# Kernel tuning notes

Hardware: AMD Instinct MI355X
Metric: run time of the kernel (lower is better)

The kernel has to match this reference:

```python
import jax, jax.numpy as jnp
import numpy as np

B, C, H, W = 4, 256, 64, 64
HALF = C // 2
BN_EPS = 1e-5


def setup_inputs() -> dict:
    key = jax.random.key(0)
    ks = jax.random.split(key, 6)
    scale = 1.0 / np.sqrt(C)
    return {
        "x": jax.random.normal(ks[0], (B, C, H, W), dtype=jnp.float32),
        "w1": jax.random.normal(ks[1], (HALF, C), dtype=jnp.float32) * scale,
        "w2": jax.random.normal(ks[2], (HALF, C), dtype=jnp.float32) * scale,
        "w3": jax.random.normal(ks[3], (HALF, C), dtype=jnp.float32) * scale,
        "w4": jax.random.normal(ks[4], (C, HALF), dtype=jnp.float32) * (1.0 / np.sqrt(HALF)),
        "gamma": jnp.ones((C,), dtype=jnp.float32),
        "beta": jnp.zeros((C,), dtype=jnp.float32),
        "running_mean": jnp.zeros((C,), dtype=jnp.float32),
        "running_var": jnp.ones((C,), dtype=jnp.float32),
    }


def _conv1x1(x, w):
    # x: [b,c,h,w], w: [out,in] -> [b,out,h,w]
    return jnp.einsum('bchw,oc->bohw', x, w)


def reference(x, w1, w2, w3, w4, gamma, beta, running_mean, running_var):
    b, Cin, h, w = x.shape
    c = Cin // 2
    hw = h * w
    n1 = _conv1x1(x, w1)  # [b,c,h,w]
    n2 = _conv1x1(x, w2)
    n3 = _conv1x1(x, w3)
    # Faithful to torch .view (raw reshape, NOT a transpose)
    q = n1.reshape(b, hw, c)   # [b,hw,c]
    k = n2.reshape(b, c, hw)   # [b,c,hw]
    attn = jnp.einsum('bic,bcj->bij', q, k)        # [b,hw,hw]
    attn = jax.nn.softmax(attn, axis=-1)
    v = n3.reshape(b, hw, c)
    res = jnp.einsum('bij,bjc->bic', attn, v)      # [b,hw,c]
    res = res.reshape(b, c, h, w)
    out = _conv1x1(res, w4)                        # [b,C,h,w]
    # BatchNorm2d in eval mode with running stats
    inv = jax.lax.rsqrt(running_var + BN_EPS)
    out = (out - running_mean[None, :, None, None]) * (gamma * inv)[None, :, None, None] + beta[None, :, None, None]
    return out + x
```

## Files before the change

### kernel.cpp

```cpp
#include <hip/hip_runtime.h>
#include <cstdint>

#define BN 4
#define CIN 256
#define HALFC 128
#define HW 4096
#define SPLIT 4
#define JT 64
#define JITERS (HW / SPLIT / JT)

typedef float  floatx4 __attribute__((ext_vector_type(4)));
typedef short  shortx8 __attribute__((ext_vector_type(8)));

#if __has_builtin(__builtin_amdgcn_exp2f)
#define EXP2F(x) __builtin_amdgcn_exp2f(x)
#else
#define EXP2F(x) exp2f(x)
#endif
#define L2E 1.44269504088896f

__device__ __forceinline__ unsigned short f2bf(float f) {
  unsigned u = __float_as_uint(f);
  u += 0x7FFFu + ((u >> 16) & 1u);
  return (unsigned short)(u >> 16);
}

__device__ __forceinline__ void async16(const void* g, void* l) {
  __builtin_amdgcn_global_load_lds((const __attribute__((address_space(1))) void*)g,
                                   (__attribute__((address_space(3))) void*)l, 16, 0, 0);
}

__global__ __launch_bounds__(256) void k_split(const float* __restrict__ x,
    const float* __restrict__ w1, const float* __restrict__ w2,
    const float* __restrict__ w3, unsigned short* __restrict__ Xth,
    unsigned short* __restrict__ Wh) {
  __shared__ float smf[64 * 65];
  int bid = blockIdx.x;
  int t = threadIdx.x;
  if (bid < 1024) {
    int b = bid >> 8, rem = bid & 255;
    int cit = rem >> 6, pxt = rem & 63;
    const float* src = x + (size_t)b * 1048576 + (size_t)(cit * 64) * HW + pxt * 64;
#pragma unroll
    for (int k = 0; k < 16; k++) {
      int idx = k * 256 + t;
      int r = idx >> 6, c = idx & 63;
      smf[r * 65 + c] = src[(size_t)r * HW + c];
    }
    __syncthreads();
    int prow = t >> 2, seg = t & 3;
    union { unsigned short us[16]; uint4 v[2]; } oh;
#pragma unroll
    for (int u = 0; u < 16; u++)
      oh.us[u] = f2bf(smf[(seg * 16 + u) * 65 + prow]);
    size_t dst = (size_t)b * 1048576 + (size_t)(pxt * 64 + prow) * 256 + cit * 64 + seg * 16;
    *(uint4*)(Xth + dst) = oh.v[0];
    *(uint4*)(Xth + dst + 8) = oh.v[1];
  } else {
    int bw = bid - 1024;
    int f0 = bw * 8192 + t * 32;
    const float* wsrc;
    int fo;
    if (f0 < 32768)      { wsrc = w1; fo = f0; }
    else if (f0 < 65536) { wsrc = w2; fo = f0 - 32768; }
    else                 { wsrc = w3; fo = f0 - 65536; }
    union { unsigned short us[32]; uint4 v[4]; } oh;
#pragma unroll
    for (int u = 0; u < 32; u++) oh.us[u] = f2bf(wsrc[fo + u]);
#pragma unroll
    for (int k = 0; k < 4; k++) *((uint4*)(Wh + f0) + k) = oh.v[k];
  }
}

__global__ __launch_bounds__(256) void k_projM(const unsigned short* __restrict__ Xth,
    const unsigned short* __restrict__ Wh, unsigned short* __restrict__ Q,
    unsigned short* __restrict__ Kt, unsigned short* __restrict__ n3) {
  __shared__ unsigned short XhS[4096];
  __shared__ unsigned short ES[9216];
  int bid = blockIdx.x;
  int pxt = bid & 31;
  int ct = bid >> 5;
  int b = ct / 6, cot = ct % 6;
  int px0 = pxt * 128, co0 = cot * 64;
  int t = threadIdx.x;
  int w = t >> 6, lane = t & 63, l16 = lane & 15, quad = lane >> 4;

  int myco = co0 + w * 16 + l16;
  shortx8 whf[8];
#pragma unroll
  for (int s = 0; s < 8; s++)
    whf[s] = *(const shortx8*)(Wh + (size_t)myco * 256 + s * 32 + quad * 8);
  floatx4 acc[8];
  floatx4 zf = {0.f, 0.f, 0.f, 0.f};
#pragma unroll
  for (int mt = 0; mt < 8; mt++) acc[mt] = zf;
  const unsigned short* XhB = Xth + (size_t)b * 1048576;
  int k8 = lane >> 4, pxm = lane & 15;

#pragma unroll
  for (int s = 0; s < 8; s++) {
    __syncthreads();
#pragma unroll
    for (int c2 = 0; c2 < 2; c2++) {
      int px = px0 + (c2 * 4 + w) * 16 + pxm;
      async16(XhB + (size_t)px * 256 + s * 32 + k8 * 8, (char*)XhS + c2 * 4096 + w * 1024);
    }
    __syncthreads();
#pragma unroll
    for (int mt = 0; mt < 8; mt++) {
      shortx8 ah = *(const shortx8*)((const char*)XhS + mt * 1024 + lane * 16);
      acc[mt] = __builtin_amdgcn_mfma_f32_16x16x32_bf16(ah, whf[s], acc[mt], 0, 0, 0);
    }
  }
  __syncthreads();
  if (cot < 2 || cot >= 4) {
    int co_l = w * 16 + l16;
#pragma unroll
    for (int mt = 0; mt < 8; mt++) {
      int px = mt * 16 + quad * 4;
      unsigned lo = (unsigned)f2bf(acc[mt][0]) | ((unsigned)f2bf(acc[mt][1]) << 16);
      unsigned hi = (unsigned)f2bf(acc[mt][2]) | ((unsigned)f2bf(acc[mt][3]) << 16);
      *(uint2*)(ES + co_l * 136 + px) = make_uint2(lo, hi);
    }
    __syncthreads();
    int cr = t >> 2, seg = t & 3;
    unsigned short* dstb = (cot < 2)
        ? Q  + (size_t)b * 524288 + (size_t)(co0 + cr) * HW
        : n3 + (size_t)b * 524288 + (size_t)(co0 - 256 + cr) * HW;
#pragma unroll
    for (int k2 = 0; k2 < 4; k2++) {
      uint4 v = *(const uint4*)(ES + cr * 136 + seg * 32 + k2 * 8);
      *(uint4*)(dstb + px0 + seg * 32 + k2 * 8) = v;
    }
  } else {
#pragma unroll
    for (int mt = 0; mt < 8; mt++)
#pragma unroll
      for (int rr = 0; rr < 4; rr++) {
        int px = mt * 16 + quad * 4 + rr;
        ES[px * 72 + w * 16 + l16] = f2bf(acc[mt][rr]);
      }
    __syncthreads();
    int ch0 = co0 - 128;
#pragma unroll
    for (int it = 0; it < 4; it++) {
      int cid = it * 256 + t;
      int px = cid >> 3, c8 = cid & 7;
      uint4 v = *(const uint4*)(ES + px * 72 + c8 * 8);
      *(uint4*)(Kt + (size_t)b * 524288 + (size_t)(px0 + px) * 128 + ch0 + c8 * 8) = v;
    }
  }
}

__global__ __launch_bounds__(256) void k_layoutVF(const unsigned short* __restrict__ n3,
    unsigned short* __restrict__ VtF) {
  __shared__ unsigned short sm[8192];
  int bid = blockIdx.x;
  int b = bid >> 6, jt = bid & 63;
  int t = threadIdx.x;
  const unsigned short* src = n3 + (size_t)b * 524288 + (size_t)(jt * 2) * 4096;
#pragma unroll
  for (int k = 0; k < 32; k++) sm[k * 256 + t] = src[k * 256 + t];
  __syncthreads();
  unsigned short* dst = VtF + (size_t)b * 524288 + (size_t)jt * 8192;
#pragma unroll
  for (int k = 0; k < 4; k++) {
    int s = k * 256 + t;
    int nt = s >> 7, kt = (s >> 6) & 1, quad = (s >> 4) & 3, l16 = s & 15;
    union { unsigned short us[8]; uint4 v; } o;
#pragma unroll
    for (int e = 0; e < 8; e++)
      o.us[e] = sm[kt * 4096 + (quad * 8 + e) * 128 + nt * 16 + l16];
    *(uint4*)(dst + s * 8) = o.v;
  }
}

__global__ __launch_bounds__(256, 2) void k_flash(const unsigned short* __restrict__ Q,
    const unsigned short* __restrict__ Kt, const unsigned short* __restrict__ VtF,
    float* __restrict__ Opart, float* __restrict__ ml) {
  __shared__ unsigned short KtS[2 * 8192];
  __shared__ unsigned short PS[4 * 32 * 64];
  int bid0 = blockIdx.x;
  int bid = (bid0 & 7) * 64 + (bid0 >> 3);
  int itile = bid & 31, sp = (bid >> 5) & 3, b = bid >> 7;
  int t = threadIdx.x;
  int w = t >> 6, lane = t & 63, l16 = lane & 15, quad = lane >> 4;
  int i0 = itile * 128;

  shortx8 qf[2][4];
#pragma unroll
  for (int ig = 0; ig < 2; ig++) {
    const unsigned short* qp = Q + ((size_t)b * HW + i0 + w * 32 + ig * 16 + l16) * 128 + quad * 8;
#pragma unroll
    for (int ks = 0; ks < 4; ks++) qf[ig][ks] = *(const shortx8*)(qp + ks * 32);
  }
  __asm__ __volatile__("s_waitcnt vmcnt(0)" ::: "memory");

  floatx4 O[2][8];
  floatx4 zf = {0.f, 0.f, 0.f, 0.f};
#pragma unroll
  for (int ig = 0; ig < 2; ig++)
#pragma unroll
    for (int nt = 0; nt < 8; nt++) O[ig][nt] = zf;
  float m_i[2] = {-1e30f, -1e30f}, l_i[2] = {0.f, 0.f};

  int ccK = w * 4 + quad;
  const unsigned short* kbase = Kt + (size_t)b * HW * 128
                              + (size_t)(sp * 1024 + l16) * 128 + ccK * 8;
  const unsigned short* vB = VtF + (size_t)b * 524288 + (size_t)(sp * 16) * 8192 + lane * 8;
  char* Pw = (char*)PS + w * 4096;

#pragma unroll
  for (int c4 = 0; c4 < 4; c4++)
    async16(kbase + c4 * 2048, (char*)KtS + c4 * 4096 + w * 1024);

  for (int it = 0; it < JITERS; it++) {
    int cur = it & 1, nxt = cur ^ 1;
    __asm__ __volatile__("s_barrier" ::: "memory");
    shortx8 vf[8][2];
    {
      const unsigned short* vt = vB + (size_t)it * 8192;
#pragma unroll
      for (int nt = 0; nt < 8; nt++)
#pragma unroll
        for (int kt = 0; kt < 2; kt++)
          vf[nt][kt] = *(const shortx8*)(vt + (nt * 2 + kt) * 512);
    }
    if (it + 1 < JITERS) {
      const unsigned short* kp = kbase + (size_t)(it + 1) * 8192;
#pragma unroll
      for (int c4 = 0; c4 < 4; c4++)
        async16(kp + c4 * 2048, (char*)KtS + nxt * 16384 + c4 * 4096 + w * 1024);
      __asm__ __volatile__("s_waitcnt vmcnt(20)" ::: "memory");
    } else {
      __asm__ __volatile__("s_waitcnt vmcnt(16)" ::: "memory");
    }
    __asm__ __volatile__("s_barrier" ::: "memory");

    const char* kc = (const char*)KtS + cur * 16384;

    floatx4 S[2][4];
#pragma unroll
    for (int ig = 0; ig < 2; ig++)
#pragma unroll
      for (int mt = 0; mt < 4; mt++) S[ig][mt] = zf;
    __builtin_amdgcn_s_setprio(1);
#pragma unroll
    for (int mt = 0; mt < 4; mt++) {
#pragma unroll
      for (int ks = 0; ks < 4; ks++) {
        shortx8 af = *(const shortx8*)(kc + mt * 4096 + ks * 1024 + lane * 16);
        S[0][mt] = __builtin_amdgcn_mfma_f32_16x16x32_bf16(af, qf[0][ks], S[0][mt], 0, 0, 0);
        S[1][mt] = __builtin_amdgcn_mfma_f32_16x16x32_bf16(af, qf[1][ks], S[1][mt], 0, 0, 0);
      }
    }
    __builtin_amdgcn_s_setprio(0);

    float tmax[2];
#pragma unroll
    for (int ig = 0; ig < 2; ig++) {
      float a0 = fmaxf(fmaxf(S[ig][0][0], S[ig][0][1]), fmaxf(S[ig][0][2], S[ig][0][3]));
      float a1 = fmaxf(fmaxf(S[ig][1][0], S[ig][1][1]), fmaxf(S[ig][1][2], S[ig][1][3]));
      float a2 = fmaxf(fmaxf(S[ig][2][0], S[ig][2][1]), fmaxf(S[ig][2][2], S[ig][2][3]));
      float a3 = fmaxf(fmaxf(S[ig][3][0], S[ig][3][1]), fmaxf(S[ig][3][2], S[ig][3][3]));
      float tm = fmaxf(fmaxf(a0, a1), fmaxf(a2, a3));
      tm = fmaxf(tm, __shfl_xor(tm, 16));
      tm = fmaxf(tm, __shfl_xor(tm, 32));
      tmax[ig] = tm;
    }
    float alpha[2] = {1.f, 1.f};
    if (__ballot(tmax[0] > m_i[0] + 8.f || tmax[1] > m_i[1] + 8.f)) {
#pragma unroll
      for (int ig = 0; ig < 2; ig++) {
        float mn = fmaxf(m_i[ig], tmax[ig]);
        alpha[ig] = EXP2F((m_i[ig] - mn) * L2E);
        m_i[ig] = mn;
        float ar[4];
#pragma unroll
        for (int rr = 0; rr < 4; rr++) ar[rr] = __shfl(alpha[ig], quad * 4 + rr);
#pragma unroll
        for (int nt = 0; nt < 8; nt++)
#pragma unroll
          for (int rr = 0; rr < 4; rr++) O[ig][nt][rr] *= ar[rr];
      }
    }
#pragma unroll
    for (int ig = 0; ig < 2; ig++) {
      float nsc = m_i[ig] * L2E;
      float sm[4];
#pragma unroll
      for (int mt = 0; mt < 4; mt++) {
        float p0 = EXP2F(fmaf(S[ig][mt][0], L2E, -nsc));
        float p1 = EXP2F(fmaf(S[ig][mt][1], L2E, -nsc));
        float p2 = EXP2F(fmaf(S[ig][mt][2], L2E, -nsc));
        float p3 = EXP2F(fmaf(S[ig][mt][3], L2E, -nsc));
        S[ig][mt][0] = p0; S[ig][mt][1] = p1; S[ig][mt][2] = p2; S[ig][mt][3] = p3;
        sm[mt] = (p0 + p1) + (p2 + p3);
      }
      float ts = (sm[0] + sm[1]) + (sm[2] + sm[3]);
      ts += __shfl_xor(ts, 16);
      ts += __shfl_xor(ts, 32);
      l_i[ig] = l_i[ig] * alpha[ig] + ts;
#pragma unroll
      for (int mt = 0; mt < 4; mt++) {
        unsigned lo = __builtin_amdgcn_perm(__float_as_uint(S[ig][mt][1]),
                                            __float_as_uint(S[ig][mt][0]), 0x07060302u);
        unsigned hi = __builtin_amdgcn_perm(__float_as_uint(S[ig][mt][3]),
                                            __float_as_uint(S[ig][mt][2]), 0x07060302u);
        *(uint2*)(Pw + ig * 2048 + (mt * 2 + (quad >> 1)) * 256 + l16 * 16 + (quad & 1) * 8)
            = make_uint2(lo, hi);
      }
    }
    __asm__ __volatile__("s_waitcnt lgkmcnt(0)" ::: "memory");
    if (it + 1 < JITERS) {
      __asm__ __volatile__("s_waitcnt vmcnt(4)" ::: "memory");
    } else {
      __asm__ __volatile__("s_waitcnt vmcnt(0)" ::: "memory");
    }
    __builtin_amdgcn_s_setprio(1);
#pragma unroll
    for (int kt = 0; kt < 2; kt++) {
      shortx8 pf0 = *(const shortx8*)(Pw + kt * 1024 + lane * 16);
      shortx8 pf1 = *(const shortx8*)(Pw + 2048 + kt * 1024 + lane * 16);
#pragma unroll
      for (int nt = 0; nt < 8; nt++) {
        O[0][nt] = __builtin_amdgcn_mfma_f32_16x16x32_bf16(pf0, vf[nt][kt], O[0][nt], 0, 0, 0);
        O[1][nt] = __builtin_amdgcn_mfma_f32_16x16x32_bf16(pf1, vf[nt][kt], O[1][nt], 0, 0, 0);
      }
    }
    __builtin_amdgcn_s_setprio(0);
  }
#pragma unroll
  for (int ig = 0; ig < 2; ig++) {
    float* Ob = Opart + ((size_t)(sp * 4 + b) * HW + i0 + w * 32 + ig * 16) * 128;
#pragma unroll
    for (int nt = 0; nt < 8; nt++)
#pragma unroll
      for (int rr = 0; rr < 4; rr++)
        Ob[(size_t)(quad * 4 + rr) * 128 + nt * 16 + l16] = O[ig][nt][rr];
  }
  if (quad == 0) {
    float2* mlp = (float2*)ml;
#pragma unroll
    for (int ig = 0; ig < 2; ig++)
      mlp[(size_t)(sp * 4 + b) * HW + i0 + w * 32 + ig * 16 + l16]
          = make_float2(m_i[ig], l_i[ig]);
  }
}

__global__ __launch_bounds__(256) void k_merge(const float* __restrict__ Opart,
    const float* __restrict__ ml, float* __restrict__ res) {
  size_t e = (size_t)blockIdx.x * 256 + threadIdx.x;
  int cq = (int)(e & 31);
  int i = (int)((e >> 5) & 4095);
  int b = (int)(e >> 17);
  const float2* mlp = (const float2*)ml;
  float m[SPLIT], l[SPLIT];
  float M = -1e30f;
#pragma unroll
  for (int s = 0; s < SPLIT; s++) {
    float2 st = mlp[(size_t)(s * 4 + b) * HW + i];
    m[s] = st.x; l[s] = st.y;
    M = fmaxf(M, m[s]);
  }
  float denom = 0.f;
  float wgt[SPLIT];
#pragma unroll
  for (int s = 0; s < SPLIT; s++) {
    float ws_ = EXP2F((m[s] - M) * L2E);
    wgt[s] = ws_;
    denom += l[s] * ws_;
  }
  float inv = 1.f / denom;
  floatx4 acc = {0.f, 0.f, 0.f, 0.f};
#pragma unroll
  for (int s = 0; s < SPLIT; s++) {
    floatx4 v = *(const floatx4*)(Opart + ((size_t)(s * 4 + b) * HW + i) * 128 + cq * 4);
    acc += v * (wgt[s] * inv);
  }
  *(floatx4*)(res + e * 4) = acc;
}

__global__ __launch_bounds__(256) void k_out(const float* __restrict__ res,
    const float* __restrict__ w4, const float* __restrict__ gamma,
    const float* __restrict__ beta, const float* __restrict__ rmean,
    const float* __restrict__ rvar, const float* __restrict__ x,
    float* __restrict__ out) {
  __shared__ float wt[16 * 128];
  int bid = blockIdx.x;
  int cot = bid & 15;
  int st = (bid >> 4) & 15;
  int b = bid >> 8;
  int t = threadIdx.x;
  int co0 = cot * 16;
#pragma unroll
  for (int k = 0; k < 8; k++) wt[k * 256 + t] = w4[(size_t)co0 * 128 + k * 256 + t];
  __syncthreads();
  int px = st * 256 + t;
  const float* rb = res + (size_t)b * 524288 + px;
  float acc[16];
#pragma unroll
  for (int r = 0; r < 16; r++) acc[r] = 0.f;
  for (int ci = 0; ci < 128; ci += 4) {
    float xv[4];
#pragma unroll
    for (int kk = 0; kk < 4; kk++) xv[kk] = rb[(size_t)(ci + kk) * HW];
#pragma unroll
    for (int r = 0; r < 16; r++) {
      floatx4 wv = *(const floatx4*)&wt[r * 128 + ci];
#pragma unroll
      for (int kk = 0; kk < 4; kk++) acc[r] += wv[kk] * xv[kk];
    }
  }
  const float* xb = x + ((size_t)b * 256 + co0) * HW + px;
  float* ob = out + ((size_t)b * 256 + co0) * HW + px;
#pragma unroll
  for (int r = 0; r < 16; r++) {
    int co = co0 + r;
    float g = gamma[co] * rsqrtf(rvar[co] + 1e-5f);
    float bb = beta[co] - rmean[co] * g;
    ob[(size_t)r * HW] = acc[r] * g + bb + xb[(size_t)r * HW];
  }
}

extern "C" void kernel_launch(void* const* d_in, const int* in_sizes, int n_in,
                              void* d_out, int out_size, void* d_ws, size_t ws_size,
                              hipStream_t stream) {
  const float* x     = (const float*)d_in[0];
  const float* w1    = (const float*)d_in[1];
  const float* w2    = (const float*)d_in[2];
  const float* w3    = (const float*)d_in[3];
  const float* w4    = (const float*)d_in[4];
  const float* gamma = (const float*)d_in[5];
  const float* beta  = (const float*)d_in[6];
  const float* rmean = (const float*)d_in[7];
  const float* rvar  = (const float*)d_in[8];
  float* out = (float*)d_out;
  char* ws = (char*)d_ws;

  size_t off = (size_t)SPLIT * 4 * HW * 128 * 4;
  float* Opart = (float*)ws;
  unsigned short* n3  = (unsigned short*)ws;
  unsigned short* Xth = (unsigned short*)(ws + ((size_t)8 << 20));
  unsigned short* Q   = (unsigned short*)(ws + off); off += (size_t)4 * HW * 128 * 2;
  unsigned short* Kt  = (unsigned short*)(ws + off); off += (size_t)4 * HW * 128 * 2;
  unsigned short* VtF = (unsigned short*)(ws + off); off += (size_t)4 * HW * 128 * 2;
  float* ml  = (float*)(ws + off); off += (size_t)SPLIT * 4 * HW * 2 * 4;
  float* res = (float*)(ws + off); off += (size_t)4 * HW * 128 * 4;
  unsigned short* Wh = (unsigned short*)(ws + off); off += (size_t)384 * 256 * 2;
  if (ws_size < off) return;

  k_split   <<<1036, 256, 0, stream>>>(x, w1, w2, w3, Xth, Wh);
  k_projM   <<<768,  256, 0, stream>>>(Xth, Wh, Q, Kt, n3);
  k_layoutVF<<<256,  256, 0, stream>>>(n3, VtF);
  k_flash   <<<512,  256, 0, stream>>>(Q, Kt, VtF, Opart, ml);
  k_merge   <<<2048, 256, 0, stream>>>(Opart, ml, res);
  k_out     <<<1024, 256, 0, stream>>>(res, w4, gamma, beta, rmean, rvar, x, out);
}
```

Measured before the change: 191.2 us.

## Software-pipeline flash loop so previous P·V MFMAs overlap current QK and softmax

Moves the body of the attention loop into an inlined helper and unrolls the loop by two. Each step now runs the P·V product for the previous key tile while the current tile's V fragments load and before its QK scores and softmax. The P tile and V register fragments are double-buffered, and a trailing P·V runs after the loop. The aim is to hide the wait on V loads and shared-memory P writes behind matrix work, at the cost of doubled V registers and extra LDS, which risks spills or lower occupancy.

Measured after the change: 200.5 us. +4.9%, slower.

```diff
diff --git a/kernel.cpp b/kernel.cpp
--- a/kernel.cpp
+++ b/kernel.cpp
@@ -175,11 +175,132 @@
   }
 }
 
+__device__ __forceinline__ void flash_body(int it, bool haspv,
+    shortx8 (&vfc)[8][2], shortx8 (&vfp)[8][2],
+    shortx8 (&qf)[2][4], floatx4 (&O)[2][8],
+    float (&m_i)[2], float (&l_i)[2],
+    const unsigned short* vB, const unsigned short* kbase,
+    unsigned short* KtS, char* Pw, int w, int lane, int l16, int quad) {
+  int cur = it & 1, nxt = cur ^ 1;
+  floatx4 zf = {0.f, 0.f, 0.f, 0.f};
+  __asm__ __volatile__("s_barrier" ::: "memory");
+  {
+    const unsigned short* vt = vB + (size_t)it * 8192;
+#pragma unroll
+    for (int nt = 0; nt < 8; nt++)
+#pragma unroll
+      for (int kt = 0; kt < 2; kt++)
+        vfc[nt][kt] = *(const shortx8*)(vt + (nt * 2 + kt) * 512);
+  }
+  if (it + 1 < JITERS) {
+    const unsigned short* kp = kbase + (size_t)(it + 1) * 8192;
+#pragma unroll
+    for (int c4 = 0; c4 < 4; c4++)
+      async16(kp + c4 * 2048, (char*)KtS + nxt * 16384 + c4 * 4096 + w * 1024);
+    __asm__ __volatile__("s_waitcnt vmcnt(20)" ::: "memory");
+  } else {
+    __asm__ __volatile__("s_waitcnt vmcnt(16)" ::: "memory");
+  }
+  __asm__ __volatile__("s_barrier" ::: "memory");
+
+  if (haspv) {
+    __asm__ __volatile__("s_waitcnt lgkmcnt(0)" ::: "memory");
+    const char* Pr = Pw + ((it ^ 1) & 1) * 4096;
+    __builtin_amdgcn_s_setprio(1);
+#pragma unroll
+    for (int kt = 0; kt < 2; kt++) {
+      shortx8 pf0 = *(const shortx8*)(Pr + kt * 1024 + lane * 16);
+      shortx8 pf1 = *(const shortx8*)(Pr + 2048 + kt * 1024 + lane * 16);
+#pragma unroll
+      for (int nt = 0; nt < 8; nt++) {
+        O[0][nt] = __builtin_amdgcn_mfma_f32_16x16x32_bf16(pf0, vfp[nt][kt], O[0][nt], 0, 0, 0);
+        O[1][nt] = __builtin_amdgcn_mfma_f32_16x16x32_bf16(pf1, vfp[nt][kt], O[1][nt], 0, 0, 0);
+      }
+    }
+    __builtin_amdgcn_s_setprio(0);
+  }
+
+  const char* kc = (const char*)KtS + cur * 16384;
+  floatx4 S[2][4];
+#pragma unroll
+  for (int ig = 0; ig < 2; ig++)
+#pragma unroll
+    for (int mt = 0; mt < 4; mt++) S[ig][mt] = zf;
+  __builtin_amdgcn_s_setprio(1);
+#pragma unroll
+  for (int mt = 0; mt < 4; mt++) {
+#pragma unroll
+    for (int ks = 0; ks < 4; ks++) {
+      shortx8 af = *(const shortx8*)(kc + mt * 4096 + ks * 1024 + lane * 16);
+      S[0][mt] = __builtin_amdgcn_mfma_f32_16x16x32_bf16(af, qf[0][ks], S[0][mt], 0, 0, 0);
+      S[1][mt] = __builtin_amdgcn_mfma_f32_16x16x32_bf16(af, qf[1][ks], S[1][mt], 0, 0, 0);
+    }
+  }
+  __builtin_amdgcn_s_setprio(0);
+
+  float tmax[2];
+#pragma unroll
+  for (int ig = 0; ig < 2; ig++) {
+    float a0 = fmaxf(fmaxf(S[ig][0][0], S[ig][0][1]), fmaxf(S[ig][0][2], S[ig][0][3]));
+    float a1 = fmaxf(fmaxf(S[ig][1][0], S[ig][1][1]), fmaxf(S[ig][1][2], S[ig][1][3]));
+    float a2 = fmaxf(fmaxf(S[ig][2][0], S[ig][2][1]), fmaxf(S[ig][2][2], S[ig][2][3]));
+    float a3 = fmaxf(fmaxf(S[ig][3][0], S[ig][3][1]), fmaxf(S[ig][3][2], S[ig][3][3]));
+    float tm = fmaxf(fmaxf(a0, a1), fmaxf(a2, a3));
+    tm = fmaxf(tm, __shfl_xor(tm, 16));
+    tm = fmaxf(tm, __shfl_xor(tm, 32));
+    tmax[ig] = tm;
+  }
+  float alpha[2] = {1.f, 1.f};
+  if (__ballot(tmax[0] > m_i[0] + 8.f || tmax[1] > m_i[1] + 8.f)) {
+#pragma unroll
+    for (int ig = 0; ig < 2; ig++) {
+      float mn = fmaxf(m_i[ig], tmax[ig]);
+      alpha[ig] = EXP2F((m_i[ig] - mn) * L2E);
+      m_i[ig] = mn;
+      float ar[4];
+#pragma unroll
+      for (int rr = 0; rr < 4; rr++) ar[rr] = __shfl(alpha[ig], quad * 4 + rr);
+#pragma unroll
+      for (int nt = 0; nt < 8; nt++)
+#pragma unroll
+        for (int rr = 0; rr < 4; rr++) O[ig][nt][rr] *= ar[rr];
+    }
+  }
+  char* Pd = Pw + (it & 1) * 4096;
+#pragma unroll
+  for (int ig = 0; ig < 2; ig++) {
+    float nsc = m_i[ig] * L2E;
+    float sm[4];
+#pragma unroll
+    for (int mt = 0; mt < 4; mt++) {
+      float p0 = EXP2F(fmaf(S[ig][mt][0], L2E, -nsc));
+      float p1 = EXP2F(fmaf(S[ig][mt][1], L2E, -nsc));
+      float p2 = EXP2F(fmaf(S[ig][mt][2], L2E, -nsc));
+      float p3 = EXP2F(fmaf(S[ig][mt][3], L2E, -nsc));
+      S[ig][mt][0] = p0; S[ig][mt][1] = p1; S[ig][mt][2] = p2; S[ig][mt][3] = p3;
+      sm[mt] = (p0 + p1) + (p2 + p3);
+    }
+    float ts = (sm[0] + sm[1]) + (sm[2] + sm[3]);
+    ts += __shfl_xor(ts, 16);
+    ts += __shfl_xor(ts, 32);
+    l_i[ig] = l_i[ig] * alpha[ig] + ts;
+#pragma unroll
+    for (int mt = 0; mt < 4; mt++) {
+      unsigned lo = __builtin_amdgcn_perm(__float_as_uint(S[ig][mt][1]),
+                                          __float_as_uint(S[ig][mt][0]), 0x07060302u);
+      unsigned hi = __builtin_amdgcn_perm(__float_as_uint(S[ig][mt][3]),
+                                          __float_as_uint(S[ig][mt][2]), 0x07060302u);
+      *(uint2*)(Pd + ig * 2048 + (mt * 2 + (quad >> 1)) * 256 + l16 * 16 + (quad & 1) * 8)
+          = make_uint2(lo, hi);
+    }
+  }
+}
+
 __global__ __launch_bounds__(256, 2) void k_flash(const unsigned short* __restrict__ Q,
     const unsigned short* __restrict__ Kt, const unsigned short* __restrict__ VtF,
     float* __restrict__ Opart, float* __restrict__ ml) {
   __shared__ unsigned short KtS[2 * 8192];
-  __shared__ unsigned short PS[4 * 32 * 64];
+  __shared__ unsigned short PS[4 * 2 * 2048];
   int bid0 = blockIdx.x;
   int bid = (bid0 & 7) * 64 + (bid0 >> 3);
   int itile = bid & 31, sp = (bid >> 5) & 3, b = bid >> 7;
@@ -208,127 +329,31 @@
   const unsigned short* kbase = Kt + (size_t)b * HW * 128
                               + (size_t)(sp * 1024 + l16) * 128 + ccK * 8;
   const unsigned short* vB = VtF + (size_t)b * 524288 + (size_t)(sp * 16) * 8192 + lane * 8;
-  char* Pw = (char*)PS + w * 4096;
+  char* Pw = (char*)PS + w * 8192;
 
 #pragma unroll
   for (int c4 = 0; c4 < 4; c4++)
     async16(kbase + c4 * 2048, (char*)KtS + c4 * 4096 + w * 1024);
 
-  for (int it = 0; it < JITERS; it++) {
-    int cur = it & 1, nxt = cur ^ 1;
-    __asm__ __volatile__("s_barrier" ::: "memory");
-    shortx8 vf[8][2];
-    {
-      const unsigned short* vt = vB + (size_t)it * 8192;
-#pragma unroll
-      for (int nt = 0; nt < 8; nt++)
-#pragma unroll
-        for (int kt = 0; kt < 2; kt++)
-          vf[nt][kt] = *(const shortx8*)(vt + (nt * 2 + kt) * 512);
-    }
-    if (it + 1 < JITERS) {
-      const unsigned short* kp = kbase + (size_t)(it + 1) * 8192;
-#pragma unroll
-      for (int c4 = 0; c4 < 4; c4++)
-        async16(kp + c4 * 2048, (char*)KtS + nxt * 16384 + c4 * 4096 + w * 1024);
-      __asm__ __volatile__("s_waitcnt vmcnt(20)" ::: "memory");
-    } else {
-      __asm__ __volatile__("s_waitcnt vmcnt(16)" ::: "memory");
-    }
-    __asm__ __volatile__("s_barrier" ::: "memory");
-
-    const char* kc = (const char*)KtS + cur * 16384;
-
-    floatx4 S[2][4];
-#pragma unroll
-    for (int ig = 0; ig < 2; ig++)
-#pragma unroll
-      for (int mt = 0; mt < 4; mt++) S[ig][mt] = zf;
-    __builtin_amdgcn_s_setprio(1);
-#pragma unroll
-    for (int mt = 0; mt < 4; mt++) {
-#pragma unroll
-      for (int ks = 0; ks < 4; ks++) {
-        shortx8 af = *(const shortx8*)(kc + mt * 4096 + ks * 1024 + lane * 16);
-        S[0][mt] = __builtin_amdgcn_mfma_f32_16x16x32_bf16(af, qf[0][ks], S[0][mt], 0, 0, 0);
-        S[1][mt] = __builtin_amdgcn_mfma_f32_16x16x32_bf16(af, qf[1][ks], S[1][mt], 0, 0, 0);
+  shortx8 vfA[8][2], vfB[8][2];
+#pragma unroll 1
+  for (int it2 = 0; it2 < JITERS; it2 += 2) {
+    flash_body(it2,     it2 > 0, vfA, vfB, qf, O, m_i, l_i, vB, kbase, KtS, Pw, w, lane, l16, quad);
+    flash_body(it2 + 1, true,    vfB, vfA, qf, O, m_i, l_i, vB, kbase, KtS, Pw, w, lane, l16, quad);
+  }
+  {
+    __asm__ __volatile__("s_waitcnt lgkmcnt(0)" ::: "memory");
+    const char* Pr = Pw + ((JITERS - 1) & 1) * 4096;
+#pragma unroll
+    for (int kt = 0; kt < 2; kt++) {
+      shortx8 pf0 = *(const shortx8*)(Pr + kt * 1024 + lane * 16);
+      shortx8 pf1 = *(const shortx8*)(Pr + 2048 + kt * 1024 + lane * 16);
+#pragma unroll
+      for (int nt = 0; nt < 8; nt++) {
+        O[0][nt] = __builtin_amdgcn_mfma_f32_16x16x32_bf16(pf0, vfB[nt][kt], O[0][nt], 0, 0, 0);
+        O[1][nt] = __builtin_amdgcn_mfma_f32_16x16x32_bf16(pf1, vfB[nt][kt], O[1][nt], 0, 0, 0);
       }
     }
-    __builtin_amdgcn_s_setprio(0);
-
-    float tmax[2];
-#pragma unroll
-    for (int ig = 0; ig < 2; ig++) {
-      float a0 = fmaxf(fmaxf(S[ig][0][0], S[ig][0][1]), fmaxf(S[ig][0][2], S[ig][0][3]));
-      float a1 = fmaxf(fmaxf(S[ig][1][0], S[ig][1][1]), fmaxf(S[ig][1][2], S[ig][1][3]));
-      float a2 = fmaxf(fmaxf(S[ig][2][0], S[ig][2][1]), fmaxf(S[ig][2][2], S[ig][2][3]));
-      float a3 = fmaxf(fmaxf(S[ig][3][0], S[ig][3][1]), fmaxf(S[ig][3][2], S[ig][3][3]));
-      float tm = fmaxf(fmaxf(a0, a1), fmaxf(a2, a3));
-      tm = fmaxf(tm, __shfl_xor(tm, 16));
-      tm = fmaxf(tm, __shfl_xor(tm, 32));
-      tmax[ig] = tm;
-    }
-    float alpha[2] = {1.f, 1.f};
-    if (__ballot(tmax[0] > m_i[0] + 8.f || tmax[1] > m_i[1] + 8.f)) {
-#pragma unroll
-      for (int ig = 0; ig < 2; ig++) {
-        float mn = fmaxf(m_i[ig], tmax[ig]);
-        alpha[ig] = EXP2F((m_i[ig] - mn) * L2E);
-        m_i[ig] = mn;
-        float ar[4];
-#pragma unroll
-        for (int rr = 0; rr < 4; rr++) ar[rr] = __shfl(alpha[ig], quad * 4 + rr);
-#pragma unroll
-        for (int nt = 0; nt < 8; nt++)
-#pragma unroll
-          for (int rr = 0; rr < 4; rr++) O[ig][nt][rr] *= ar[rr];
-      }
-    }
-#pragma unroll
-    for (int ig = 0; ig < 2; ig++) {
-      float nsc = m_i[ig] * L2E;
-      float sm[4];
-#pragma unroll
-      for (int mt = 0; mt < 4; mt++) {
-        float p0 = EXP2F(fmaf(S[ig][mt][0], L2E, -nsc));
-        float p1 = EXP2F(fmaf(S[ig][mt][1], L2E, -nsc));
-        float p2 = EXP2F(fmaf(S[ig][mt][2], L2E, -nsc));
-        float p3 = EXP2F(fmaf(S[ig][mt][3], L2E, -nsc));
-        S[ig][mt][0] = p0; S[ig][mt][1] = p1; S[ig][mt][2] = p2; S[ig][mt][3] = p3;
-        sm[mt] = (p0 + p1) + (p2 + p3);
-      }
-      float ts = (sm[0] + sm[1]) + (sm[2] + sm[3]);
-      ts += __shfl_xor(ts, 16);
-      ts += __shfl_xor(ts, 32);
-      l_i[ig] = l_i[ig] * alpha[ig] + ts;
-#pragma unroll
-      for (int mt = 0; mt < 4; mt++) {
-        unsigned lo = __builtin_amdgcn_perm(__float_as_uint(S[ig][mt][1]),
-                                            __float_as_uint(S[ig][mt][0]), 0x07060302u);
-        unsigned hi = __builtin_amdgcn_perm(__float_as_uint(S[ig][mt][3]),
-                                            __float_as_uint(S[ig][mt][2]), 0x07060302u);
-        *(uint2*)(Pw + ig * 2048 + (mt * 2 + (quad >> 1)) * 256 + l16 * 16 + (quad & 1) * 8)
-            = make_uint2(lo, hi);
-      }
-    }
-    __asm__ __volatile__("s_waitcnt lgkmcnt(0)" ::: "memory");
-    if (it + 1 < JITERS) {
-      __asm__ __volatile__("s_waitcnt vmcnt(4)" ::: "memory");
-    } else {
-      __asm__ __volatile__("s_waitcnt vmcnt(0)" ::: "memory");
-    }
-    __builtin_amdgcn_s_setprio(1);
-#pragma unroll
-    for (int kt = 0; kt < 2; kt++) {
-      shortx8 pf0 = *(const shortx8*)(Pw + kt * 1024 + lane * 16);
-      shortx8 pf1 = *(const shortx8*)(Pw + 2048 + kt * 1024 + lane * 16);
-#pragma unroll
-      for (int nt = 0; nt < 8; nt++) {
-        O[0][nt] = __builtin_amdgcn_mfma_f32_16x16x32_bf16(pf0, vf[nt][kt], O[0][nt], 0, 0, 0);
-        O[1][nt] = __builtin_amdgcn_mfma_f32_16x16x32_bf16(pf1, vf[nt][kt], O[1][nt], 0, 0, 0);
-      }
-    }
-    __builtin_amdgcn_s_setprio(0);
   }
 #pragma unroll
   for (int ig = 0; ig < 2; ig++) {
```

## Fuse all stages into one cooperative persistent kernel with grid syncs

Applied to the files above, without the earlier changes.

Refactors each stage kernel body into a device function and adds a cooperative megakernel that runs all six stages in a 512-block grid, separated by grid-wide barriers and sharing one LDS buffer. The aim is to remove the launch gaps and tail drain between the six kernel launches. The trade-off is that every stage is now held to 2 blocks per CU with 48KB of LDS, and the grid barriers add their own cost. If occupancy is too low or the cooperative launch fails, it falls back to the separate launches.

Result: no change. 191.7 us (+0.3%).

```diff
diff --git a/kernel.cpp b/kernel.cpp
--- a/kernel.cpp
+++ b/kernel.cpp
@@ -1,5 +1,8 @@
 #include <hip/hip_runtime.h>
+#include <hip/hip_cooperative_groups.h>
 #include <cstdint>
+
+namespace cg = cooperative_groups;
 
 #define BN 4
 #define CIN 256
@@ -30,15 +33,13 @@
                                    (__attribute__((address_space(3))) void*)l, 16, 0, 0);
 }
 
-__global__ __launch_bounds__(256) void k_split(const float* __restrict__ x,
-    const float* __restrict__ w1, const float* __restrict__ w2,
-    const float* __restrict__ w3, unsigned short* __restrict__ Xth,
-    unsigned short* __restrict__ Wh) {
-  __shared__ float smf[64 * 65];
-  int bid = blockIdx.x;
-  int t = threadIdx.x;
-  if (bid < 1024) {
-    int b = bid >> 8, rem = bid & 255;
+
+__device__ __forceinline__ void body_split(int vb, int t, float* smf,
+    const float* __restrict__ x, const float* __restrict__ w1,
+    const float* __restrict__ w2, const float* __restrict__ w3,
+    unsigned short* __restrict__ Xth, unsigned short* __restrict__ Wh) {
+  if (vb < 1024) {
+    int b = vb >> 8, rem = vb & 255;
     int cit = rem >> 6, pxt = rem & 63;
     const float* src = x + (size_t)b * 1048576 + (size_t)(cit * 64) * HW + pxt * 64;
 #pragma unroll
@@ -57,7 +58,7 @@
     *(uint4*)(Xth + dst) = oh.v[0];
     *(uint4*)(Xth + dst + 8) = oh.v[1];
   } else {
-    int bw = bid - 1024;
+    int bw = vb - 1024;
     int f0 = bw * 8192 + t * 32;
     const float* wsrc;
     int fo;
@@ -72,17 +73,15 @@
   }
 }
 
-__global__ __launch_bounds__(256) void k_projM(const unsigned short* __restrict__ Xth,
-    const unsigned short* __restrict__ Wh, unsigned short* __restrict__ Q,
-    unsigned short* __restrict__ Kt, unsigned short* __restrict__ n3) {
-  __shared__ unsigned short XhS[4096];
-  __shared__ unsigned short ES[9216];
-  int bid = blockIdx.x;
-  int pxt = bid & 31;
-  int ct = bid >> 5;
+__device__ __forceinline__ void body_projM(int vb, int t,
+    unsigned short* XhS , unsigned short* ES ,
+    const unsigned short* __restrict__ Xth, const unsigned short* __restrict__ Wh,
+    unsigned short* __restrict__ Q, unsigned short* __restrict__ Kt,
+    unsigned short* __restrict__ n3) {
+  int pxt = vb & 31;
+  int ct = vb >> 5;
   int b = ct / 6, cot = ct % 6;
   int px0 = pxt * 128, co0 = cot * 64;
-  int t = threadIdx.x;
   int w = t >> 6, lane = t & 63, l16 = lane & 15, quad = lane >> 4;
 
   int myco = co0 + w * 16 + l16;
@@ -152,12 +151,9 @@
   }
 }
 
-__global__ __launch_bounds__(256) void k_layoutVF(const unsigned short* __restrict__ n3,
-    unsigned short* __restrict__ VtF) {
-  __shared__ unsigned short sm[8192];
-  int bid = blockIdx.x;
-  int b = bid >> 6, jt = bid & 63;
-  int t = threadIdx.x;
+__device__ __forceinline__ void body_layoutVF(int vb, int t, unsigned short* sm,
+    const unsigned short* __restrict__ n3, unsigned short* __restrict__ VtF) {
+  int b = vb >> 6, jt = vb & 63;
   const unsigned short* src = n3 + (size_t)b * 524288 + (size_t)(jt * 2) * 4096;
 #pragma unroll
   for (int k = 0; k < 32; k++) sm[k * 256 + t] = src[k * 256 + t];
@@ -175,15 +171,13 @@
   }
 }
 
-__global__ __launch_bounds__(256, 2) void k_flash(const unsigned short* __restrict__ Q,
-    const unsigned short* __restrict__ Kt, const unsigned short* __restrict__ VtF,
-    float* __restrict__ Opart, float* __restrict__ ml) {
-  __shared__ unsigned short KtS[2 * 8192];
-  __shared__ unsigned short PS[4 * 32 * 64];
-  int bid0 = blockIdx.x;
+__device__ __forceinline__ void body_flash(int bid0, int t,
+    unsigned short* KtS , unsigned short* PS ,
+    const unsigned short* __restrict__ Q, const unsigned short* __restrict__ Kt,
+    const unsigned short* __restrict__ VtF, float* __restrict__ Opart,
+    float* __restrict__ ml) {
   int bid = (bid0 & 7) * 64 + (bid0 >> 3);
   int itile = bid & 31, sp = (bid >> 5) & 3, b = bid >> 7;
-  int t = threadIdx.x;
   int w = t >> 6, lane = t & 63, l16 = lane & 15, quad = lane >> 4;
   int i0 = itile * 128;
 
@@ -230,7 +224,7 @@
       const unsigned short* kp = kbase + (size_t)(it + 1) * 8192;
 #pragma unroll
       for (int c4 = 0; c4 < 4; c4++)
-        async16(kp + c4 * 2048, (char*)KtS + nxt * 16384 + c4 * 4096 + w * 1024);
+        async16(kp + c4 * 2048, (char*)KtS + nxt * 8192 * 2 + c4 * 4096 + w * 1024);
       __asm__ __volatile__("s_waitcnt vmcnt(20)" ::: "memory");
     } else {
       __asm__ __volatile__("s_waitcnt vmcnt(16)" ::: "memory");
@@ -348,9 +342,10 @@
   }
 }
 
-__global__ __launch_bounds__(256) void k_merge(const float* __restrict__ Opart,
-    const float* __restrict__ ml, float* __restrict__ res) {
-  size_t e = (size_t)blockIdx.x * 256 + threadIdx.x;
+__device__ __forceinline__ void body_merge(int vb, int t,
+    const float* __restrict__ Opart, const float* __restrict__ ml,
+    float* __restrict__ res) {
+  size_t e = (size_t)vb * 256 + t;
   int cq = (int)(e & 31);
   int i = (int)((e >> 5) & 4095);
   int b = (int)(e >> 17);
@@ -381,45 +376,136 @@
   *(floatx4*)(res + e * 4) = acc;
 }
 
+__device__ __forceinline__ void body_out(int vb, int t, float* wt ,
+    const float* __restrict__ res, const float* __restrict__ w4,
+    const float* __restrict__ gamma, const float* __restrict__ beta,
+    const float* __restrict__ rmean, const float* __restrict__ rvar,
+    const float* __restrict__ x, float* __restrict__ out) {
+  int cot = vb & 15;
+  int st = (vb >> 4) & 15;
+  int b = vb >> 8;
+  int co0 = cot * 16;
+#pragma unroll
+  for (int k = 0; k < 8; k++) wt[k * 256 + t] = w4[(size_t)co0 * 128 + k * 256 + t];
+  __syncthreads();
+  int px = st * 256 + t;
+  const float* rb = res + (size_t)b * 524288 + px;
+  float acc[16];
+#pragma unroll
+  for (int r = 0; r < 16; r++) acc[r] = 0.f;
+  for (int ci = 0; ci < 128; ci += 4) {
+    float xv[4];
+#pragma unroll
+    for (int kk = 0; kk < 4; kk++) xv[kk] = rb[(size_t)(ci + kk) * HW];
+#pragma unroll
+    for (int r = 0; r < 16; r++) {
+      floatx4 wv = *(const floatx4*)&wt[r * 128 + ci];
+#pragma unroll
+      for (int kk = 0; kk < 4; kk++) acc[r] += wv[kk] * xv[kk];
+    }
+  }
+  const float* xb = x + ((size_t)b * 256 + co0) * HW + px;
+  float* ob = out + ((size_t)b * 256 + co0) * HW + px;
+#pragma unroll
+  for (int r = 0; r < 16; r++) {
+    int co = co0 + r;
+    float g = gamma[co] * rsqrtf(rvar[co] + 1e-5f);
+    float bb = beta[co] - rmean[co] * g;
+    ob[(size_t)r * HW] = acc[r] * g + bb + xb[(size_t)r * HW];
+  }
+}
+
+
+__global__ __launch_bounds__(256) void k_split(const float* __restrict__ x,
+    const float* __restrict__ w1, const float* __restrict__ w2,
+    const float* __restrict__ w3, unsigned short* __restrict__ Xth,
+    unsigned short* __restrict__ Wh) {
+  __shared__ float smf[64 * 65];
+  body_split(blockIdx.x, threadIdx.x, smf, x, w1, w2, w3, Xth, Wh);
+}
+
+__global__ __launch_bounds__(256) void k_projM(const unsigned short* __restrict__ Xth,
+    const unsigned short* __restrict__ Wh, unsigned short* __restrict__ Q,
+    unsigned short* __restrict__ Kt, unsigned short* __restrict__ n3) {
+  __shared__ unsigned short XhS[4096];
+  __shared__ unsigned short ES[9216];
+  body_projM(blockIdx.x, threadIdx.x, XhS, ES, Xth, Wh, Q, Kt, n3);
+}
+
+__global__ __launch_bounds__(256) void k_layoutVF(const unsigned short* __restrict__ n3,
+    unsigned short* __restrict__ VtF) {
+  __shared__ unsigned short sm[8192];
+  body_layoutVF(blockIdx.x, threadIdx.x, sm, n3, VtF);
+}
+
+__global__ __launch_bounds__(256, 2) void k_flash(const unsigned short* __restrict__ Q,
+    const unsigned short* __restrict__ Kt, const unsigned short* __restrict__ VtF,
+    float* __restrict__ Opart, float* __restrict__ ml) {
+  __shared__ unsigned short KtS[2 * 8192];
+  __shared__ unsigned short PS[4 * 32 * 64];
+  body_flash(blockIdx.x, threadIdx.x, KtS, PS, Q, Kt, VtF, Opart, ml);
+}
+
+__global__ __launch_bounds__(256) void k_merge(const float* __restrict__ Opart,
+    const float* __restrict__ ml, float* __restrict__ res) {
+  body_merge(blockIdx.x, threadIdx.x, Opart, ml, res);
+}
+
 __global__ __launch_bounds__(256) void k_out(const float* __restrict__ res,
     const float* __restrict__ w4, const float* __restrict__ gamma,
     const float* __restrict__ beta, const float* __restrict__ rmean,
     const float* __restrict__ rvar, const float* __restrict__ x,
     float* __restrict__ out) {
   __shared__ float wt[16 * 128];
+  body_out(blockIdx.x, threadIdx.x, wt, res, w4, gamma, beta, rmean, rvar, x, out);
+}
+
+__global__ __launch_bounds__(256, 2) void k_mega(
+    const float* __restrict__ x, const float* __restrict__ w1,
+    const float* __restrict__ w2, const float* __restrict__ w3,
+    const float* __restrict__ w4, const float* __restrict__ gamma,
+    const float* __restrict__ beta, const float* __restrict__ rmean,
+    const float* __restrict__ rvar, float* __restrict__ out,
+    unsigned short* __restrict__ Xth, unsigned short* __restrict__ Wh,
+    unsigned short* __restrict__ Q, unsigned short* __restrict__ Kt,
+    unsigned short* __restrict__ n3, unsigned short* __restrict__ VtF,
+    float* __restrict__ Opart, float* __restrict__ ml, float* __restrict__ res) {
+  cg::grid_group grid = cg::this_grid();
+  __shared__ __align__(16) char smem[49152];
+  int t = threadIdx.x;
   int bid = blockIdx.x;
-  int cot = bid & 15;
-  int st = (bid >> 4) & 15;
-  int b = bid >> 8;
-  int t = threadIdx.x;
-  int co0 = cot * 16;
-#pragma unroll
-  for (int k = 0; k < 8; k++) wt[k * 256 + t] = w4[(size_t)co0 * 128 + k * 256 + t];
+
+  for (int vb = bid; vb < 1036; vb += 512) {
+    __syncthreads();
+    body_split(vb, t, (float*)smem, x, w1, w2, w3, Xth, Wh);
+  }
+  grid.sync();
+
+  for (int vb = bid; vb < 768; vb += 512) {
+    __syncthreads();
+    body_projM(vb, t, (unsigned short*)smem, (unsigned short*)(smem + 8192),
+               Xth, Wh, Q, Kt, n3);
+  }
+  grid.sync();
+
+  for (int vb = bid; vb < 256; vb += 512) {
+    __syncthreads();
+    body_layoutVF(vb, t, (unsigned short*)smem, n3, VtF);
+  }
+  grid.sync();
+
   __syncthreads();
-  int px = st * 256 + t;
-  const float* rb = res + (size_t)b * 524288 + px;
-  float acc[16];
-#pragma unroll
-  for (int r = 0; r < 16; r++) acc[r] = 0.f;
-  for (int ci = 0; ci < 128; ci += 4) {
-    float xv[4];
-#pragma unroll
-    for (int kk = 0; kk < 4; kk++) xv[kk] = rb[(size_t)(ci + kk) * HW];
-#pragma unroll
-    for (int r = 0; r < 16; r++) {
-      floatx4 wv = *(const floatx4*)&wt[r * 128 + ci];
-#pragma unroll
-      for (int kk = 0; kk < 4; kk++) acc[r] += wv[kk] * xv[kk];
-    }
-  }
-  const float* xb = x + ((size_t)b * 256 + co0) * HW + px;
-  float* ob = out + ((size_t)b * 256 + co0) * HW + px;
-#pragma unroll
-  for (int r = 0; r < 16; r++) {
-    int co = co0 + r;
-    float g = gamma[co] * rsqrtf(rvar[co] + 1e-5f);
-    float bb = beta[co] - rmean[co] * g;
-    ob[(size_t)r * HW] = acc[r] * g + bb + xb[(size_t)r * HW];
+  body_flash(bid, t, (unsigned short*)smem, (unsigned short*)(smem + 32768),
+             Q, Kt, VtF, Opart, ml);
+  grid.sync();
+
+  for (int vb = bid; vb < 2048; vb += 512)
+    body_merge(vb, t, Opart, ml, res);
+  grid.sync();
+
+  for (int vb = bid; vb < 1024; vb += 512) {
+    __syncthreads();
+    body_out(vb, t, (float*)smem, res, w4, gamma, beta, rmean, rvar, x, out);
   }
 }
 
@@ -450,6 +536,24 @@
   unsigned short* Wh = (unsigned short*)(ws + off); off += (size_t)384 * 256 * 2;
   if (ws_size < off) return;
 
+  static int coop = -1;
+  if (coop < 0) {
+    int nb = 0;
+    hipError_t e = hipOccupancyMaxActiveBlocksPerMultiprocessor(
+        &nb, (const void*)k_mega, 256, 0);
+    coop = (e == hipSuccess && nb >= 2) ? 1 : 0;
+  }
+  if (coop == 1) {
+    void* args[] = {(void*)&x, (void*)&w1, (void*)&w2, (void*)&w3, (void*)&w4,
+                    (void*)&gamma, (void*)&beta, (void*)&rmean, (void*)&rvar,
+                    (void*)&out, (void*)&Xth, (void*)&Wh, (void*)&Q, (void*)&Kt,
+                    (void*)&n3, (void*)&VtF, (void*)&Opart, (void*)&ml, (void*)&res};
+    hipError_t e = hipLaunchCooperativeKernel((const void*)k_mega, dim3(512),
+                                              dim3(256), args, 0, stream);
+    if (e == hipSuccess) return;
+    coop = 0;
+  }
+
   k_split   <<<1036, 256, 0, stream>>>(x, w1, w2, w3, Xth, Wh);
   k_projM   <<<768,  256, 0, stream>>>(Xth, Wh, Q, Kt, n3);
   k_layoutVF<<<256,  256, 0, stream>>>(n3, VtF);
```

## Stage V tiles through LDS and software-pipeline PV MFMA with next QK

Applied to the files above, without the earlier changes.

V tiles were loaded directly into registers from global memory each iteration. They are now async-copied into a double-buffered LDS region. The P·V matmul for iteration it-1 is deferred into iteration it and interleaved with the QK^T MFMAs, with a final epilogue handling the last tile. This is meant to overlap softmax and exp work with matrix-core work and to cut register pressure from the vf array. In exchange it adds LDS traffic, an extra barrier per iteration and larger shared memory use, which could reduce occupancy.

Measured after the change: 186.5 us. 2.4% less time.

```diff
diff --git a/kernel.cpp b/kernel.cpp
--- a/kernel.cpp
+++ b/kernel.cpp
@@ -179,7 +179,8 @@
     const unsigned short* __restrict__ Kt, const unsigned short* __restrict__ VtF,
     float* __restrict__ Opart, float* __restrict__ ml) {
   __shared__ unsigned short KtS[2 * 8192];
-  __shared__ unsigned short PS[4 * 32 * 64];
+  __shared__ unsigned short VS[2 * 8192];
+  __shared__ unsigned short PS[4 * 2048];
   int bid0 = blockIdx.x;
   int bid = (bid0 & 7) * 64 + (bid0 >> 3);
   int itile = bid & 31, sp = (bid >> 5) & 3, b = bid >> 7;
@@ -207,37 +208,32 @@
   int ccK = w * 4 + quad;
   const unsigned short* kbase = Kt + (size_t)b * HW * 128
                               + (size_t)(sp * 1024 + l16) * 128 + ccK * 8;
-  const unsigned short* vB = VtF + (size_t)b * 524288 + (size_t)(sp * 16) * 8192 + lane * 8;
+  const unsigned short* vbase = VtF + (size_t)b * 524288 + (size_t)(sp * 16) * 8192
+                              + w * 512 + lane * 8;
   char* Pw = (char*)PS + w * 4096;
 
 #pragma unroll
-  for (int c4 = 0; c4 < 4; c4++)
+  for (int c4 = 0; c4 < 4; c4++) {
     async16(kbase + c4 * 2048, (char*)KtS + c4 * 4096 + w * 1024);
+    async16(vbase + c4 * 2048, (char*)VS + c4 * 4096 + w * 1024);
+  }
 
   for (int it = 0; it < JITERS; it++) {
     int cur = it & 1, nxt = cur ^ 1;
-    __asm__ __volatile__("s_barrier" ::: "memory");
-    shortx8 vf[8][2];
-    {
-      const unsigned short* vt = vB + (size_t)it * 8192;
-#pragma unroll
-      for (int nt = 0; nt < 8; nt++)
-#pragma unroll
-        for (int kt = 0; kt < 2; kt++)
-          vf[nt][kt] = *(const shortx8*)(vt + (nt * 2 + kt) * 512);
-    }
     if (it + 1 < JITERS) {
       const unsigned short* kp = kbase + (size_t)(it + 1) * 8192;
 #pragma unroll
       for (int c4 = 0; c4 < 4; c4++)
         async16(kp + c4 * 2048, (char*)KtS + nxt * 16384 + c4 * 4096 + w * 1024);
-      __asm__ __volatile__("s_waitcnt vmcnt(20)" ::: "memory");
+      __asm__ __volatile__("s_waitcnt vmcnt(4)" ::: "memory");
     } else {
-      __asm__ __volatile__("s_waitcnt vmcnt(16)" ::: "memory");
+      __asm__ __volatile__("s_waitcnt vmcnt(0)" ::: "memory");
     }
     __asm__ __volatile__("s_barrier" ::: "memory");
+    __asm__ __volatile__("s_waitcnt lgkmcnt(0)" ::: "memory");
 
     const char* kc = (const char*)KtS + cur * 16384;
+    const char* vc = (const char*)VS + cur * 16384;
 
     floatx4 S[2][4];
 #pragma unroll
@@ -245,6 +241,20 @@
 #pragma unroll
       for (int mt = 0; mt < 4; mt++) S[ig][mt] = zf;
     __builtin_amdgcn_s_setprio(1);
+    if (it > 0) {
+      const char* vp = (const char*)VS + nxt * 16384;
+#pragma unroll
+      for (int kt = 0; kt < 2; kt++) {
+        shortx8 pf0 = *(const shortx8*)(Pw + kt * 1024 + lane * 16);
+        shortx8 pf1 = *(const shortx8*)(Pw + 2048 + kt * 1024 + lane * 16);
+#pragma unroll
+        for (int nt = 0; nt < 8; nt++) {
+          shortx8 vfr = *(const shortx8*)(vp + ((nt * 2 + kt) * 64 + lane) * 16);
+          O[0][nt] = __builtin_amdgcn_mfma_f32_16x16x32_bf16(pf0, vfr, O[0][nt], 0, 0, 0);
+          O[1][nt] = __builtin_amdgcn_mfma_f32_16x16x32_bf16(pf1, vfr, O[1][nt], 0, 0, 0);
+        }
+      }
+    }
 #pragma unroll
     for (int mt = 0; mt < 4; mt++) {
 #pragma unroll
@@ -255,6 +265,13 @@
       }
     }
     __builtin_amdgcn_s_setprio(0);
+    __asm__ __volatile__("s_barrier" ::: "memory");
+    if (it + 1 < JITERS) {
+      const unsigned short* vp2 = vbase + (size_t)(it + 1) * 8192;
+#pragma unroll
+      for (int c4 = 0; c4 < 4; c4++)
+        async16(vp2 + c4 * 2048, (char*)VS + nxt * 16384 + c4 * 4096 + w * 1024);
+    }
 
     float tmax[2];
 #pragma unroll
@@ -311,24 +328,21 @@
             = make_uint2(lo, hi);
       }
     }
-    __asm__ __volatile__("s_waitcnt lgkmcnt(0)" ::: "memory");
-    if (it + 1 < JITERS) {
-      __asm__ __volatile__("s_waitcnt vmcnt(4)" ::: "memory");
-    } else {
-      __asm__ __volatile__("s_waitcnt vmcnt(0)" ::: "memory");
-    }
-    __builtin_amdgcn_s_setprio(1);
+  }
+  __asm__ __volatile__("s_waitcnt lgkmcnt(0)" ::: "memory");
+  {
+    const char* vp = (const char*)VS + ((JITERS - 1) & 1) * 16384;
 #pragma unroll
     for (int kt = 0; kt < 2; kt++) {
       shortx8 pf0 = *(const shortx8*)(Pw + kt * 1024 + lane * 16);
       shortx8 pf1 = *(const shortx8*)(Pw + 2048 + kt * 1024 + lane * 16);
 #pragma unroll
       for (int nt = 0; nt < 8; nt++) {
-        O[0][nt] = __builtin_amdgcn_mfma_f32_16x16x32_bf16(pf0, vf[nt][kt], O[0][nt], 0, 0, 0);
-        O[1][nt] = __builtin_amdgcn_mfma_f32_16x16x32_bf16(pf1, vf[nt][kt], O[1][nt], 0, 0, 0);
-      }
-    }
-    __builtin_amdgcn_s_setprio(0);
+        shortx8 vfr = *(const shortx8*)(vp + ((nt * 2 + kt) * 64 + lane) * 16);
+        O[0][nt] = __builtin_amdgcn_mfma_f32_16x16x32_bf16(pf0, vfr, O[0][nt], 0, 0, 0);
+        O[1][nt] = __builtin_amdgcn_mfma_f32_16x16x32_bf16(pf1, vfr, O[1][nt], 0, 0, 0);
+      }
+    }
   }
 #pragma unroll
   for (int ig = 0; ig < 2; ig++) {
```
